# Kernel optimization log

Hardware: AMD Instinct MI355X
Metric: run time of the kernel (lower is better)

## Reference

```python
import jax, jax.numpy as jnp
import numpy as np

B, T, H, LAT, ADIM = 8192, 40, 100, 10, 2
ATT_TEMP = 5.0


def setup_inputs() -> dict:
    key = jax.random.key(0)
    ks = jax.random.split(key, 12)
    return {
        "sampled_att_z": jax.random.normal(ks[0], (B, LAT), jnp.float32),
        "enc_h": jax.random.normal(ks[1], (B, H), jnp.float32),
        # keep IDM params strictly positive / physically plausible to avoid inf
        "idm_params": 1.0 + 2.0 * jax.random.uniform(ks[2], (B, 5), jnp.float32),
        "idm_s": jax.random.uniform(ks[3], (B, T, 8), jnp.float32),
        "sdv_acts": jax.random.normal(ks[4], (B, T, ADIM), jnp.float32),
        "linear_W": jax.random.normal(ks[5], (LAT, H), jnp.float32) / np.float32(np.sqrt(LAT)),
        "linear_b": jnp.zeros((H,), jnp.float32),
        "lstm_Wx": jax.random.normal(ks[6], (H + ADIM, 4 * H), jnp.float32) / np.float32(np.sqrt(H + ADIM)),
        "lstm_Wh": jax.random.normal(ks[7], (H, 4 * H), jnp.float32) / np.float32(np.sqrt(H)),
        "lstm_b": jnp.zeros((4 * H,), jnp.float32),
        "att_W": jax.random.normal(ks[8], (H, 1), jnp.float32) / np.float32(np.sqrt(H)),
        "att_b": jnp.zeros((1,), jnp.float32),
        # precomputed per-step noise, replacing tf.random.normal inside the loop
        "noise_f": jax.random.normal(ks[9], (T, B, 1), jnp.float32),
        "noise_m": jax.random.normal(ks[10], (T, B, 1), jnp.float32),
    }


def reference(sampled_att_z, enc_h, idm_params, idm_s, sdv_acts,
              linear_W, linear_b, lstm_Wx, lstm_Wh, lstm_b, att_W, att_b,
              noise_f, noise_m):
    desired_v = idm_params[:, 0:1]
    desired_tgap = idm_params[:, 1:2]
    min_jamx = idm_params[:, 2:3]
    max_act = idm_params[:, 3:4]
    min_act = idm_params[:, 4:5]

    def idm_driver(vel, dv, dx):  # all [B,1]
        dx = jnp.clip(dx, 0.5, 1000.0)
        desired_gap = min_jamx + jax.nn.relu(
            desired_tgap * vel + vel * dv / (2.0 * jnp.sqrt(max_act * min_act)))
        act = max_act * (1.0 - (vel / desired_v) ** 4 - (desired_gap / dx) ** 2)
        return jnp.clip(act, -3.0, 3.0)

    att_proj = sampled_att_z @ linear_W + linear_b  # [B,H]; also the att_context and init h,c

    s_tm = jnp.swapaxes(idm_s, 0, 1)      # [T,B,8]
    a_tm = jnp.swapaxes(sdv_acts, 0, 1)   # [T,B,ADIM]

    ego_v0 = idm_s[:, 0, 0:1]
    ego_x0 = idm_s[:, 0, 3:4]
    zero_act = jnp.zeros_like(ego_v0)  # step-0 kinematic update is a no-op

    def step(carry, xs):
        ego_v, ego_x, h, c, act = carry
        s, sdv, nf, nm = xs
        ego_v = ego_v + act * 0.1
        ego_x = ego_x + ego_v * 0.1 + 0.5 * act * 0.1 ** 2

        f_v, m_v = s[:, 1:2], s[:, 2:3]
        f_x, m_x = s[:, 4:5], s[:, 5:6]
        f_ex, m_ex = s[:, 6:7], s[:, 7:8]

        ef_act = idm_driver(ego_v, ego_v - f_v, f_x - ego_x)
        ef_act = f_ex * ef_act + (1.0 - f_ex) * nf
        em_act = idm_driver(ego_v, ego_v - m_v, m_x - ego_x)
        em_act = m_ex * em_act + (1.0 - m_ex) * nm

        x_in = jnp.concatenate([att_proj, sdv], axis=-1)  # [B,H+ADIM]
        z = x_in @ lstm_Wx + h @ lstm_Wh + lstm_b          # [B,4H], keras gate order i,f,g,o
        zi, zf, zg, zo = jnp.split(z, 4, axis=-1)
        c = jax.nn.sigmoid(zf) * c + jax.nn.sigmoid(zi) * jnp.tanh(zg)
        h = jax.nn.sigmoid(zo) * jnp.tanh(c)

        att_score = jax.nn.sigmoid(ATT_TEMP * (h @ att_W + att_b))  # [B,1]
        act = (1.0 - att_score) * ef_act + att_score * em_act
        return (ego_v, ego_x, h, c, act), (act, att_score)

    init = (ego_v0, ego_x0, att_proj, att_proj, zero_act)
    _, (acts, atts) = jax.lax.scan(step, init, (s_tm, a_tm, noise_f, noise_m))
    act_seq = jnp.swapaxes(acts, 0, 1)  # [B,T,1]
    att_seq = jnp.swapaxes(atts, 0, 1)  # [B,T,1]
    return act_seq, att_seq
```

## Files before the change

### kernel.cpp

```cpp
#include <hip/hip_runtime.h>
#include <math.h>


#define B_TOT 8192
#define T_STEPS 40
#define NB 16

typedef _Float16 f16;
typedef f16 f16x8 __attribute__((ext_vector_type(8)));
typedef float f32x4 __attribute__((ext_vector_type(4)));

__device__ __forceinline__ float rcpf(float x) { return __builtin_amdgcn_rcpf(x); }
__device__ __forceinline__ float ex2(float x)  { return __builtin_amdgcn_exp2f(x); }
__device__ __forceinline__ float sigf(float x)  { return rcpf(1.f + ex2(-1.44269504f * x)); }


__global__ __launch_bounds__(256) void idm_prep(
    const float* __restrict__ Wx, const float* __restrict__ Wh,
    const float* __restrict__ bvec, const float* __restrict__ attw,
    const float* __restrict__ attB,
    f16* __restrict__ whb, f16* __restrict__ wxb,
    float* __restrict__ bp)
{
  int i = blockIdx.x * 256 + threadIdx.x;
  int k = i >> 9, n = i & 511;
  int g = n >> 7, j128 = n & 127;
  float sc = (g == 2) ? 2.88539008f : 1.44269504f;
  float vh = 0.f, vx = 0.f;
  if (j128 < 100) {
    int col = g * 100 + j128;
    if (k < 100)      { vh = Wh[k * 400 + col] * sc; vx = Wx[k * 400 + col] * sc; }
    else if (k < 102) { vh = Wx[k * 400 + col] * sc; }
  } else if (n == 100 && k < 100) {
    vh = attw[k];
  }
  int idx = (((n >> 4) * 4 + (k >> 5)) * 64 + (((k >> 3) & 3) * 16 + (n & 15))) * 8 + (k & 7);
  whb[idx] = (f16)vh;
  wxb[idx] = (f16)vx;
  if (i < 512) {
    int gg = i >> 7, jj = i & 127;
    float scb = (gg == 2) ? 2.88539008f : 1.44269504f;
    bp[i] = (jj < 100) ? bvec[gg * 100 + jj] * scb
                       : ((i == 100) ? attB[0] : 0.f);
  }
}

#define MM(z, a, g, kf) z = __builtin_amdgcn_mfma_f32_16x16x32_f16(a, wb[g][kf], z, 0, 0, 0)

#define TAIL_STEP(tt) {                                                        \
    int tt_ = (tt);                                                            \
    float inv_dv = pS[0][l], des_tg = pS[1][l], min_jx = pS[2][l];             \
    float max_a = pS[3][l], inv2s = pS[4][l];                                  \
    float2 s01 = *(const float2*)&sS[l][tt_][0];                               \
    float2 s23 = *(const float2*)&sS[l][tt_][2];                               \
    float2 s45 = *(const float2*)&sS[l][tt_][4];                               \
    float nf = nS[0][tt_][l], nm = nS[1][tt_][l];                              \
    float lg = logitS[tt_][l];                                                 \
    ego_v += actT * 0.1f;                                                      \
    ego_x += ego_v * 0.1f + actT * 0.005f;                                     \
    float dxf = fminf(fmaxf(s23.x - ego_x, 0.5f), 1000.f);                     \
    float dgf = min_jx + fmaxf(0.f, des_tg * ego_v + ego_v * (ego_v - s01.x) * inv2s); \
    float rr = ego_v * inv_dv; float rr2 = rr * rr;                            \
    float qf = dgf * rcpf(dxf);                                                \
    float af_ = fminf(fmaxf(max_a * (1.f - rr2 * rr2 - qf * qf), -3.f), 3.f);  \
    float dxm = fminf(fmaxf(s23.y - ego_x, 0.5f), 1000.f);                     \
    float dgm = min_jx + fmaxf(0.f, des_tg * ego_v + ego_v * (ego_v - s01.y) * inv2s); \
    float qm = dgm * rcpf(dxm);                                                \
    float am_ = fminf(fmaxf(max_a * (1.f - rr2 * rr2 - qm * qm), -3.f), 3.f);  \
    float ef2 = s45.x * af_ + (1.f - s45.x) * nf;                              \
    float em2 = s45.y * am_ + (1.f - s45.y) * nm;                              \
    float att = sigf(5.f * lg);                                                \
    actT = (1.f - att) * ef2 + att * em2;                                      \
    accS[0][l][tt_] = actT;                                                    \
    accS[1][l][tt_] = att;                                                     \
  }

__global__ __launch_bounds__(448, 4) void idm_main(
    const float* __restrict__ z_att,
    const float* __restrict__ linear_W,
    const float* __restrict__ linear_b,
    const float* __restrict__ sdv_acts,
    const f16* __restrict__ whb, const f16* __restrict__ wxb,
    const float* __restrict__ bp,
    const float* __restrict__ idm_params,
    const float* __restrict__ idm_s,
    const float* __restrict__ noise_f,
    const float* __restrict__ noise_m,
    float* __restrict__ out)
{
  __shared__ f16   hS[2][16][136];
  __shared__ f16   sdvS[T_STEPS][16][2];
  __shared__ float logitS[T_STEPS][16];
  __shared__ float sS[16][T_STEPS][6];
  __shared__ float nS[2][T_STEPS][16];
  __shared__ float accS[2][16][T_STEPS];
  __shared__ float pS[5][16];

  const int tid = threadIdx.x;
  const int w  = tid >> 6;
  const int l  = tid & 63;
  const int lr = l & 15;
  const int lq = l >> 4;
  const int b0g = blockIdx.x * NB;
  const int jcol = 16 * w + lr;
  const bool tail_lane = (tid < NB);

  for (int idx = tid; idx < 2176; idx += 448) ((unsigned*)hS)[idx] = 0u;
  for (int idx = tid; idx < 1280; idx += 448) {
    float v = sdv_acts[(size_t)b0g * 80 + idx];
    int b = idx / 80, r = idx - b * 80;
    sdvS[r >> 1][b][r & 1] = (f16)v;
  }
  for (int idx = tid; idx < 5120; idx += 448) {
    int f = idx & 7;
    if (f != 0 && f != 3) {
      int b = idx / 320, rem = idx - b * 320, t = rem >> 3;
      sS[b][t][(f < 3) ? f - 1 : f - 2] = idm_s[(size_t)b0g * 320 + idx];
    }
  }
  for (int idx = tid; idx < 1280; idx += 448) {
    int which = idx >= 640 ? 1 : 0;
    int r = idx - which * 640;
    int t = r >> 4, i = r & 15;
    nS[which][t][i] = which ? noise_m[(size_t)t * B_TOT + b0g + i]
                            : noise_f[(size_t)t * B_TOT + b0g + i];
  }
  if (tid < 80) pS[tid % 5][tid / 5] = idm_params[(size_t)b0g * 5 + tid];
  __syncthreads();

  if (tid < 16) {
    pS[0][tid] = rcpf(pS[0][tid]);
    pS[4][tid] = 0.5f / sqrtf(pS[3][tid] * pS[4][tid]);
  }

  if (tid >= 64 && tid < 320) {
    int s2 = tid - 64;
    int b = s2 >> 4, oct = s2 & 15;
    float za[10];
    #pragma unroll
    for (int t2 = 0; t2 < 10; ++t2) za[t2] = z_att[(b0g + b) * 10 + t2];
    #pragma unroll
    for (int jj = 0; jj < 8; ++jj) {
      int j = oct * 8 + jj;
      if (j < 100) {
        float acc = linear_b[j];
        #pragma unroll
        for (int t2 = 0; t2 < 10; ++t2) acc = fmaf(za[t2], linear_W[t2 * 100 + j], acc);
        hS[0][b][j] = (f16)acc;
      }
    }
  }
  if (tid < 32) hS[0][tid >> 1][100 + (tid & 1)] = sdvS[0][tid >> 1][tid & 1];
  __syncthreads();

  f16x8 wb[4][4];
  #pragma unroll
  for (int g = 0; g < 4; ++g) {
    int tile = w + 8 * g;
    #pragma unroll
    for (int kf = 0; kf < 4; ++kf)
      wb[g][kf] = *(const f16x8*)(wxb + ((size_t)(tile * 4 + kf) * 64 + l) * 8);
  }
  f32x4 cx[4];
  #pragma unroll
  for (int g = 0; g < 4; ++g) {
    float bpv = bp[(w + 8 * g) * 16 + lr];
    f32x4 c = {bpv, bpv, bpv, bpv};
    cx[g] = c;
  }
  #pragma unroll
  for (int kf = 0; kf < 4; ++kf) {
    f16x8 a = *(const f16x8*)(&hS[0][lr][kf * 32 + lq * 8]);
    #pragma unroll
    for (int g = 0; g < 4; ++g)
      cx[g] = __builtin_amdgcn_mfma_f32_16x16x32_f16(a, wb[g][kf], cx[g], 0, 0, 0);
  }
  #pragma unroll
  for (int g = 0; g < 4; ++g) {
    int tile = w + 8 * g;
    #pragma unroll
    for (int kf = 0; kf < 4; ++kf)
      wb[g][kf] = *(const f16x8*)(whb + ((size_t)(tile * 4 + kf) * 64 + l) * 8);
  }

  float cst[4];
  #pragma unroll
  for (int r = 0; r < 4; ++r) cst[r] = (float)hS[0][lq * 4 + r][jcol];

  float ego_v = 0.f, ego_x = 0.f, actT = 0.f;
  if (tail_lane) {
    ego_v = idm_s[(size_t)(b0g + l) * 320 + 0];
    ego_x = idm_s[(size_t)(b0g + l) * 320 + 3];
  }

  int p = 0;
  for (int t = 0; t < T_STEPS; ++t) {
    f16x8 a0 = *(const f16x8*)(&hS[p][lr][0  + lq * 8]);
    f16x8 a1 = *(const f16x8*)(&hS[p][lr][32 + lq * 8]);
    f16x8 a2 = *(const f16x8*)(&hS[p][lr][64 + lq * 8]);
    f16x8 a3 = *(const f16x8*)(&hS[p][lr][96 + lq * 8]);
    f32x4 z0 = cx[0], z1 = cx[1], z2 = cx[2], z3 = cx[3];
    __builtin_amdgcn_s_setprio(1);
    MM(z0,a0,0,0); MM(z1,a0,1,0); MM(z2,a0,2,0); MM(z3,a0,3,0);
    MM(z0,a1,0,1); MM(z1,a1,1,1); MM(z2,a1,2,1); MM(z3,a1,3,1);
    MM(z0,a2,0,2); MM(z1,a2,1,2); MM(z2,a2,2,2); MM(z3,a2,3,2);
    MM(z0,a3,0,3); MM(z1,a3,1,3); MM(z2,a3,2,3); MM(z3,a3,3,3);
    __builtin_amdgcn_s_setprio(0);

    if (w == 6 && t > 0 && lr == 4) {
      #pragma unroll
      for (int r = 0; r < 4; ++r) logitS[t - 1][lq * 4 + r] = z0[r];
    }

    #pragma unroll
    for (int r = 0; r < 4; ++r) {
      float e0 = ex2(-z0[r]);
      float e1 = ex2(-z1[r]);
      float e2 = fminf(ex2(z2[r]), 1e30f);
      float e3 = ex2(-z3[r]);
      float sf  = rcpf(1.f + e1);
      float itg = (e2 - 1.f) * rcpf((1.f + e0) * (1.f + e2));
      float cc  = fmaf(sf, cst[r], itg);
      float d   = fminf(ex2(2.88539008f * cc), 1e30f);
      float hh  = (d - 1.f) * rcpf((1.f + e3) * (1.f + d));
      cst[r] = cc;
      if (jcol < 100) hS[p ^ 1][lq * 4 + r][jcol] = (f16)hh;
    }
    if (t + 1 < T_STEPS && tid >= 64 && tid < 96) {
      int ll = tid - 64;
      hS[p ^ 1][ll >> 1][100 + (ll & 1)] = sdvS[t + 1][ll >> 1][ll & 1];
    }
    if (tail_lane && t >= 2) TAIL_STEP(t - 2);
    __syncthreads();
    p ^= 1;
  }

  if (w == 6) {
    float bpv6 = bp[96 + lr];
    f32x4 zL = {bpv6, bpv6, bpv6, bpv6};
    #pragma unroll
    for (int kf = 0; kf < 4; ++kf) {
      f16x8 a = *(const f16x8*)(&hS[p][lr][kf * 32 + lq * 8]);
      zL = __builtin_amdgcn_mfma_f32_16x16x32_f16(a, wb[0][kf], zL, 0, 0, 0);
    }
    if (lr == 4) {
      #pragma unroll
      for (int r = 0; r < 4; ++r) logitS[T_STEPS - 1][lq * 4 + r] = zL[r];
    }
  }
  if (tail_lane) TAIL_STEP(T_STEPS - 2);
  __syncthreads();
  if (tail_lane) TAIL_STEP(T_STEPS - 1);
  __syncthreads();

  if (tid < 160) {
    f32x4 va = ((const f32x4*)&accS[0][0][0])[tid];
    f32x4 vt = ((const f32x4*)&accS[1][0][0])[tid];
    *(f32x4*)(out + (size_t)b0g * T_STEPS + tid * 4) = va;
    *(f32x4*)(out + (size_t)B_TOT * T_STEPS + (size_t)b0g * T_STEPS + tid * 4) = vt;
  }
}

extern "C" void kernel_launch(void* const* d_in, const int* in_sizes, int n_in,
                              void* d_out, int out_size, void* d_ws, size_t ws_size,
                              hipStream_t stream) {
  const float* z_att      = (const float*)d_in[0];
  const float* idm_params = (const float*)d_in[2];
  const float* idm_s      = (const float*)d_in[3];
  const float* sdv_acts   = (const float*)d_in[4];
  const float* linear_W   = (const float*)d_in[5];
  const float* linear_b   = (const float*)d_in[6];
  const float* lstm_Wx    = (const float*)d_in[7];
  const float* lstm_Wh    = (const float*)d_in[8];
  const float* lstm_b     = (const float*)d_in[9];
  const float* att_W      = (const float*)d_in[10];
  const float* att_b      = (const float*)d_in[11];
  const float* noise_f    = (const float*)d_in[12];
  const float* noise_m    = (const float*)d_in[13];
  float* out = (float*)d_out;

  f16*   whb = (f16*)d_ws;
  f16*   wxb = (f16*)((char*)d_ws + 131072);
  float* bp  = (float*)((char*)d_ws + 262144);

  idm_prep<<<256, 256, 0, stream>>>(lstm_Wx, lstm_Wh, lstm_b, att_W, att_b,
                                    whb, wxb, bp);
  idm_main<<<B_TOT / NB, 448, 0, stream>>>(z_att, linear_W, linear_b, sdv_acts,
                                           whb, wxb, bp,
                                           idm_params, idm_s,
                                           noise_f, noise_m, out);
}
```

Before: 179.2 us.

## Move IDM tail and sdv staging into a dedicated eighth wavefront

Adds an eighth wave per block (512 threads) that does no matrix work and instead runs the scalar IDM tail step and copies the next sdv inputs into shared memory. The seven MFMA waves no longer carry the tail lanes' serial work on their critical path. Tail state now lives in shared memory rather than registers. The setprio calls around the MFMA sequence are dropped. This costs an extra wave's occupancy slot per block and adds shared-memory traffic for the tail state.

```diff
diff --git a/kernel.cpp b/kernel.cpp
--- a/kernel.cpp
+++ b/kernel.cpp
@@ -75,7 +75,13 @@
     accS[1][l][tt_] = att;                                                     \
   }
 
-__global__ __launch_bounds__(448, 4) void idm_main(
+#define TAIL_RUN(tt) {                                                         \
+    float ego_v = tS[0][l], ego_x = tS[1][l], actT = tS[2][l];                 \
+    TAIL_STEP(tt);                                                             \
+    tS[0][l] = ego_v; tS[1][l] = ego_x; tS[2][l] = actT;                       \
+  }
+
+__global__ __launch_bounds__(512, 4) void idm_main(
     const float* __restrict__ z_att,
     const float* __restrict__ linear_W,
     const float* __restrict__ linear_b,
@@ -95,6 +101,7 @@
   __shared__ float nS[2][T_STEPS][16];
   __shared__ float accS[2][16][T_STEPS];
   __shared__ float pS[5][16];
+  __shared__ float tS[3][16];
 
   const int tid = threadIdx.x;
   const int w  = tid >> 6;
@@ -103,22 +110,22 @@
   const int lq = l >> 4;
   const int b0g = blockIdx.x * NB;
   const int jcol = 16 * w + lr;
-  const bool tail_lane = (tid < NB);
-
-  for (int idx = tid; idx < 2176; idx += 448) ((unsigned*)hS)[idx] = 0u;
-  for (int idx = tid; idx < 1280; idx += 448) {
+  const bool tail_lane = (w == 7) && (l < 16);
+
+  for (int idx = tid; idx < 2176; idx += 512) ((unsigned*)hS)[idx] = 0u;
+  for (int idx = tid; idx < 1280; idx += 512) {
     float v = sdv_acts[(size_t)b0g * 80 + idx];
     int b = idx / 80, r = idx - b * 80;
     sdvS[r >> 1][b][r & 1] = (f16)v;
   }
-  for (int idx = tid; idx < 5120; idx += 448) {
+  for (int idx = tid; idx < 5120; idx += 512) {
     int f = idx & 7;
     if (f != 0 && f != 3) {
       int b = idx / 320, rem = idx - b * 320, t = rem >> 3;
       sS[b][t][(f < 3) ? f - 1 : f - 2] = idm_s[(size_t)b0g * 320 + idx];
     }
   }
-  for (int idx = tid; idx < 1280; idx += 448) {
+  for (int idx = tid; idx < 1280; idx += 512) {
     int which = idx >= 640 ? 1 : 0;
     int r = idx - which * 640;
     int t = r >> 4, i = r & 15;
@@ -131,6 +138,9 @@
   if (tid < 16) {
     pS[0][tid] = rcpf(pS[0][tid]);
     pS[4][tid] = 0.5f / sqrtf(pS[3][tid] * pS[4][tid]);
+    tS[0][tid] = idm_s[(size_t)(b0g + tid) * 320 + 0];
+    tS[1][tid] = idm_s[(size_t)(b0g + tid) * 320 + 3];
+    tS[2][tid] = 0.f;
   }
 
   if (tid >= 64 && tid < 320) {
@@ -154,83 +164,79 @@
   __syncthreads();
 
   f16x8 wb[4][4];
-  #pragma unroll
-  for (int g = 0; g < 4; ++g) {
-    int tile = w + 8 * g;
-    #pragma unroll
-    for (int kf = 0; kf < 4; ++kf)
-      wb[g][kf] = *(const f16x8*)(wxb + ((size_t)(tile * 4 + kf) * 64 + l) * 8);
-  }
   f32x4 cx[4];
-  #pragma unroll
-  for (int g = 0; g < 4; ++g) {
-    float bpv = bp[(w + 8 * g) * 16 + lr];
-    f32x4 c = {bpv, bpv, bpv, bpv};
-    cx[g] = c;
-  }
-  #pragma unroll
-  for (int kf = 0; kf < 4; ++kf) {
-    f16x8 a = *(const f16x8*)(&hS[0][lr][kf * 32 + lq * 8]);
-    #pragma unroll
-    for (int g = 0; g < 4; ++g)
-      cx[g] = __builtin_amdgcn_mfma_f32_16x16x32_f16(a, wb[g][kf], cx[g], 0, 0, 0);
-  }
-  #pragma unroll
-  for (int g = 0; g < 4; ++g) {
-    int tile = w + 8 * g;
-    #pragma unroll
-    for (int kf = 0; kf < 4; ++kf)
-      wb[g][kf] = *(const f16x8*)(whb + ((size_t)(tile * 4 + kf) * 64 + l) * 8);
-  }
-
   float cst[4];
-  #pragma unroll
-  for (int r = 0; r < 4; ++r) cst[r] = (float)hS[0][lq * 4 + r][jcol];
-
-  float ego_v = 0.f, ego_x = 0.f, actT = 0.f;
-  if (tail_lane) {
-    ego_v = idm_s[(size_t)(b0g + l) * 320 + 0];
-    ego_x = idm_s[(size_t)(b0g + l) * 320 + 3];
+  if (w < 7) {
+    #pragma unroll
+    for (int g = 0; g < 4; ++g) {
+      int tile = w + 8 * g;
+      #pragma unroll
+      for (int kf = 0; kf < 4; ++kf)
+        wb[g][kf] = *(const f16x8*)(wxb + ((size_t)(tile * 4 + kf) * 64 + l) * 8);
+    }
+    #pragma unroll
+    for (int g = 0; g < 4; ++g) {
+      float bpv = bp[(w + 8 * g) * 16 + lr];
+      f32x4 c = {bpv, bpv, bpv, bpv};
+      cx[g] = c;
+    }
+    #pragma unroll
+    for (int kf = 0; kf < 4; ++kf) {
+      f16x8 a = *(const f16x8*)(&hS[0][lr][kf * 32 + lq * 8]);
+      #pragma unroll
+      for (int g = 0; g < 4; ++g)
+        cx[g] = __builtin_amdgcn_mfma_f32_16x16x32_f16(a, wb[g][kf], cx[g], 0, 0, 0);
+    }
+    #pragma unroll
+    for (int g = 0; g < 4; ++g) {
+      int tile = w + 8 * g;
+      #pragma unroll
+      for (int kf = 0; kf < 4; ++kf)
+        wb[g][kf] = *(const f16x8*)(whb + ((size_t)(tile * 4 + kf) * 64 + l) * 8);
+    }
+    #pragma unroll
+    for (int r = 0; r < 4; ++r) cst[r] = (float)hS[0][lq * 4 + r][jcol];
   }
 
   int p = 0;
   for (int t = 0; t < T_STEPS; ++t) {
-    f16x8 a0 = *(const f16x8*)(&hS[p][lr][0  + lq * 8]);
-    f16x8 a1 = *(const f16x8*)(&hS[p][lr][32 + lq * 8]);
-    f16x8 a2 = *(const f16x8*)(&hS[p][lr][64 + lq * 8]);
-    f16x8 a3 = *(const f16x8*)(&hS[p][lr][96 + lq * 8]);
-    f32x4 z0 = cx[0], z1 = cx[1], z2 = cx[2], z3 = cx[3];
-    __builtin_amdgcn_s_setprio(1);
-    MM(z0,a0,0,0); MM(z1,a0,1,0); MM(z2,a0,2,0); MM(z3,a0,3,0);
-    MM(z0,a1,0,1); MM(z1,a1,1,1); MM(z2,a1,2,1); MM(z3,a1,3,1);
-    MM(z0,a2,0,2); MM(z1,a2,1,2); MM(z2,a2,2,2); MM(z3,a2,3,2);
-    MM(z0,a3,0,3); MM(z1,a3,1,3); MM(z2,a3,2,3); MM(z3,a3,3,3);
-    __builtin_amdgcn_s_setprio(0);
-
-    if (w == 6 && t > 0 && lr == 4) {
-      #pragma unroll
-      for (int r = 0; r < 4; ++r) logitS[t - 1][lq * 4 + r] = z0[r];
-    }
-
-    #pragma unroll
-    for (int r = 0; r < 4; ++r) {
-      float e0 = ex2(-z0[r]);
-      float e1 = ex2(-z1[r]);
-      float e2 = fminf(ex2(z2[r]), 1e30f);
-      float e3 = ex2(-z3[r]);
-      float sf  = rcpf(1.f + e1);
-      float itg = (e2 - 1.f) * rcpf((1.f + e0) * (1.f + e2));
-      float cc  = fmaf(sf, cst[r], itg);
-      float d   = fminf(ex2(2.88539008f * cc), 1e30f);
-      float hh  = (d - 1.f) * rcpf((1.f + e3) * (1.f + d));
-      cst[r] = cc;
-      if (jcol < 100) hS[p ^ 1][lq * 4 + r][jcol] = (f16)hh;
-    }
-    if (t + 1 < T_STEPS && tid >= 64 && tid < 96) {
-      int ll = tid - 64;
-      hS[p ^ 1][ll >> 1][100 + (ll & 1)] = sdvS[t + 1][ll >> 1][ll & 1];
-    }
-    if (tail_lane && t >= 2) TAIL_STEP(t - 2);
+    if (w < 7) {
+      f16x8 a0 = *(const f16x8*)(&hS[p][lr][0  + lq * 8]);
+      f16x8 a1 = *(const f16x8*)(&hS[p][lr][32 + lq * 8]);
+      f16x8 a2 = *(const f16x8*)(&hS[p][lr][64 + lq * 8]);
+      f16x8 a3 = *(const f16x8*)(&hS[p][lr][96 + lq * 8]);
+      f32x4 z0 = cx[0], z1 = cx[1], z2 = cx[2], z3 = cx[3];
+      MM(z0,a0,0,0); MM(z1,a0,1,0); MM(z2,a0,2,0); MM(z3,a0,3,0);
+      MM(z0,a1,0,1); MM(z1,a1,1,1); MM(z2,a1,2,1); MM(z3,a1,3,1);
+      MM(z0,a2,0,2); MM(z1,a2,1,2); MM(z2,a2,2,2); MM(z3,a2,3,2);
+      MM(z0,a3,0,3); MM(z1,a3,1,3); MM(z2,a3,2,3); MM(z3,a3,3,3);
+
+      if (w == 6 && t > 0 && lr == 4) {
+        #pragma unroll
+        for (int r = 0; r < 4; ++r) logitS[t - 1][lq * 4 + r] = z0[r];
+      }
+
+      #pragma unroll
+      for (int r = 0; r < 4; ++r) {
+        float e0 = ex2(-z0[r]);
+        float e1 = ex2(-z1[r]);
+        float e2 = fminf(ex2(z2[r]), 1e30f);
+        float e3 = ex2(-z3[r]);
+        float sf  = rcpf(1.f + e1);
+        float itg = (e2 - 1.f) * rcpf((1.f + e0) * (1.f + e2));
+        float cc  = fmaf(sf, cst[r], itg);
+        float d   = fminf(ex2(2.88539008f * cc), 1e30f);
+        float hh  = (d - 1.f) * rcpf((1.f + e3) * (1.f + d));
+        cst[r] = cc;
+        if (jcol < 100) hS[p ^ 1][lq * 4 + r][jcol] = (f16)hh;
+      }
+    } else {
+      if (t + 1 < T_STEPS && l >= 32) {
+        int ll = l - 32;
+        hS[p ^ 1][ll >> 1][100 + (ll & 1)] = sdvS[t + 1][ll >> 1][ll & 1];
+      }
+      if (l < 16 && t >= 2) TAIL_RUN(t - 2);
+    }
     __syncthreads();
     p ^= 1;
   }
@@ -248,9 +254,9 @@
       for (int r = 0; r < 4; ++r) logitS[T_STEPS - 1][lq * 4 + r] = zL[r];
     }
   }
-  if (tail_lane) TAIL_STEP(T_STEPS - 2);
-  __syncthreads();
-  if (tail_lane) TAIL_STEP(T_STEPS - 1);
+  if (tail_lane) TAIL_RUN(T_STEPS - 2);
+  __syncthreads();
+  if (tail_lane) TAIL_RUN(T_STEPS - 1);
   __syncthreads();
 
   if (tid < 160) {
@@ -285,7 +291,7 @@
 
   idm_prep<<<256, 256, 0, stream>>>(lstm_Wx, lstm_Wh, lstm_b, att_W, att_b,
                                     whb, wxb, bp);
-  idm_main<<<B_TOT / NB, 448, 0, stream>>>(z_att, linear_W, linear_b, sdv_acts,
+  idm_main<<<B_TOT / NB, 512, 0, stream>>>(z_att, linear_W, linear_b, sdv_acts,
                                            whb, wxb, bp,
                                            idm_params, idm_s,
                                            noise_f, noise_m, out);
```

Result: faster. 172.5 us (-3.8%).
